# Optimization experiments

Measured on AMD Instinct MI355X. Metric: run time of the kernel, lower is better.

## Reference

```python
import jax, jax.numpy as jnp
import numpy as np


def _sepconv1x1(x, dw, pw, b):
    # SeparableConv2D with kernel=1: depthwise 1x1 = per-channel scale, then pointwise matmul
    return jnp.einsum('nhwc,cd->nhwd', x * dw, pw) + b


def setup_inputs() -> dict:
    key = jax.random.key(0)
    ks = jax.random.split(key, 12)
    N, H, W, C_in, C_red = 4, 64, 64, 256, 64
    s = 0.05  # small init so softmax logits are well-conditioned
    return {
        'feature_maps': jax.random.normal(ks[0], (N, H, W, C_in), jnp.float32),
        'global_channel_output': jax.random.normal(ks[1], (N, H, W, C_in), jnp.float32),
        'dw_q': jax.random.normal(ks[2], (C_in,), jnp.float32) * s,
        'pw_q': jax.random.normal(ks[3], (C_in, C_red), jnp.float32) * s,
        'b_q': jnp.zeros((C_red,), jnp.float32),
        'dw_k': jax.random.normal(ks[4], (C_in,), jnp.float32) * s,
        'pw_k': jax.random.normal(ks[5], (C_in, C_red), jnp.float32) * s,
        'b_k': jnp.zeros((C_red,), jnp.float32),
        'dw_v': jax.random.normal(ks[6], (C_in,), jnp.float32) * s,
        'pw_v': jax.random.normal(ks[7], (C_in, C_red), jnp.float32) * s,
        'b_v': jnp.zeros((C_red,), jnp.float32),
        'dw_a': jax.random.normal(ks[8], (C_red,), jnp.float32) * s,
        'pw_a': jax.random.normal(ks[9], (C_red, C_in), jnp.float32) * s,
        'b_a': jnp.zeros((C_in,), jnp.float32),
    }


def reference(feature_maps, global_channel_output,
              dw_q, pw_q, b_q, dw_k, pw_k, b_k, dw_v, pw_v, b_v,
              dw_a, pw_a, b_a):
    N, H, W, _ = feature_maps.shape
    q = _sepconv1x1(feature_maps, dw_q, pw_q, b_q)  # [N,H,W,Cr]
    k = _sepconv1x1(feature_maps, dw_k, pw_k, b_k)
    v = _sepconv1x1(feature_maps, dw_v, pw_v, b_v)
    Cr = q.shape[-1]
    q = q.reshape(N, H * W, Cr)
    k = k.reshape(N, H * W, Cr)
    v = v.reshape(N, H * W, Cr)
    # tf.matmul(key, query, transpose_b=True): scores[i,j] = key_i . query_j
    scores = jnp.einsum('nic,njc->nij', k, q)  # [N,HW,HW]
    scores = jax.nn.softmax(scores, axis=-1)
    # tf.matmul(value, scores, transpose_a=True) -> [N,Cr,HW]
    att = jnp.einsum('nic,nij->ncj', v, scores)
    # faithful raw reshape (as in the original TF code) from [N,Cr,HW] to [N,H,W,Cr]
    att = att.reshape(N, H, W, Cr)
    att = _sepconv1x1(att, dw_a, pw_a, b_a)  # [N,H,W,C_in]
    return global_channel_output * att + global_channel_output
```

## Files before the change

kernel.cpp:

```cpp
#include <hip/hip_runtime.h>
#include <hip/hip_bf16.h>

typedef __attribute__((ext_vector_type(8))) __bf16 bf16x8;
typedef __attribute__((ext_vector_type(2))) __bf16 bf16x2;
typedef __attribute__((ext_vector_type(4))) float floatx4;
typedef __attribute__((ext_vector_type(4))) unsigned short us4;
typedef __attribute__((ext_vector_type(8))) unsigned short us8;
typedef __attribute__((ext_vector_type(4))) short s16x4;
typedef __attribute__((ext_vector_type(2))) unsigned int uint2v;
typedef __attribute__((ext_vector_type(4))) unsigned int uint4v;

#define MFMA16(A, B, C) __builtin_amdgcn_mfma_f32_16x16x32_bf16((A), (B), (C), 0, 0, 0)
#define MFMA1K(A, B, C) __builtin_amdgcn_mfma_f32_16x16x16bf16_1k((A), (B), (C), 0, 0, 0)

#define LOG2E 1.44269504088896340736f

#if __has_builtin(__builtin_amdgcn_exp2f)
#define EXP2F(x) __builtin_amdgcn_exp2f(x)
#else
#define EXP2F(x) exp2f(x)
#endif

static __device__ __forceinline__ unsigned short f2bfbits(float f) {
    __hip_bfloat16 h = __float2bfloat16(f);
    union { __hip_bfloat16 h; unsigned short u; } cv;
    cv.h = h;
    return cv.u;
}
static __device__ __forceinline__ unsigned int rne32(float f) {
    unsigned int u = __builtin_bit_cast(unsigned int, f);
    return u + 0x7fffu + ((u >> 16) & 1u);
}
static __device__ __forceinline__ unsigned short rne16(float f) {
    return (unsigned short)(rne32(f) >> 16);
}

#if __has_builtin(__builtin_amdgcn_cvt_pk_bf16_f32)
static __device__ __forceinline__ s16x4 pack4(float e0, float e1, float e2, float e3) {
    bf16x2 lo = __builtin_amdgcn_cvt_pk_bf16_f32(e0, e1);
    bf16x2 hi = __builtin_amdgcn_cvt_pk_bf16_f32(e2, e3);
    uint2v u = {__builtin_bit_cast(unsigned int, lo), __builtin_bit_cast(unsigned int, hi)};
    return __builtin_bit_cast(s16x4, u);
}
static __device__ __forceinline__ bf16x8 cvt8(floatx4 a, floatx4 b) {
    bf16x2 p0 = __builtin_amdgcn_cvt_pk_bf16_f32(a[0], a[1]);
    bf16x2 p1 = __builtin_amdgcn_cvt_pk_bf16_f32(a[2], a[3]);
    bf16x2 p2 = __builtin_amdgcn_cvt_pk_bf16_f32(b[0], b[1]);
    bf16x2 p3 = __builtin_amdgcn_cvt_pk_bf16_f32(b[2], b[3]);
    uint4v u = {__builtin_bit_cast(unsigned int, p0), __builtin_bit_cast(unsigned int, p1),
                __builtin_bit_cast(unsigned int, p2), __builtin_bit_cast(unsigned int, p3)};
    return __builtin_bit_cast(bf16x8, u);
}
#else
static __device__ __forceinline__ s16x4 pack4(float e0, float e1, float e2, float e3) {
    unsigned int pa = __builtin_amdgcn_perm(rne32(e1), rne32(e0), 0x07060302u);
    unsigned int pb = __builtin_amdgcn_perm(rne32(e3), rne32(e2), 0x07060302u);
    uint2v u = {pa, pb};
    return __builtin_bit_cast(s16x4, u);
}
static __device__ __forceinline__ bf16x8 cvt8(floatx4 a, floatx4 b) {
    us8 u;
#pragma unroll
    for (int i = 0; i < 4; i++) { u[i] = rne16(a[i]); u[4 + i] = rne16(b[i]); }
    return __builtin_bit_cast(bf16x8, u);
}
#endif

static __device__ __forceinline__ bf16x8 load_bf8(const __hip_bfloat16* p) {
    return *reinterpret_cast<const bf16x8*>(p);
}
static __device__ __forceinline__ float bf2f(unsigned short u) {
    unsigned int w = ((unsigned int)u) << 16;
    return __builtin_bit_cast(float, w);
}


__global__ __launch_bounds__(256) void prep_w(
    const float* __restrict__ dwq, const float* __restrict__ pwq,
    const float* __restrict__ dwk, const float* __restrict__ pwk,
    const float* __restrict__ dwv, const float* __restrict__ pwv,
    __hip_bfloat16* __restrict__ wT)
{
    int idx = blockIdx.x * 256 + threadIdx.x;
    int p = idx >> 14;
    int r = idx & 16383;
    int d = r >> 8, c = r & 255;
    const float* dw = (p == 0) ? dwq : ((p == 1) ? dwk : dwv);
    const float* pw = (p == 0) ? pwq : ((p == 1) ? pwk : pwv);
    float scale = (p == 1) ? LOG2E : 1.0f;
    wT[idx] = __float2bfloat16(dw[c] * pw[c * 64 + d] * scale);
}

__global__ __launch_bounds__(256) void proj_qkv(
    const float* __restrict__ x,
    const __hip_bfloat16* __restrict__ wT,
    const float* __restrict__ bqp, const float* __restrict__ bkp,
    const float* __restrict__ bvp,
    __hip_bfloat16* __restrict__ qf, __hip_bfloat16* __restrict__ kf,
    __hip_bfloat16* __restrict__ vf)
{
    int wg = blockIdx.x * 4 + (threadIdx.x >> 6);
    int p = wg >> 10;
    int wid = wg & 1023;
    int lane = threadIdx.x & 63;
    int l15 = lane & 15, quad = lane >> 4;
    int strip = wid << 4;

    floatx4 acc[4];
#pragma unroll
    for (int t = 0; t < 4; t++) acc[t] = (floatx4){0.f, 0.f, 0.f, 0.f};

    const float* xrow = x + (strip + l15) * 256 + quad * 8;
    const __hip_bfloat16* wp = wT + p * 16384;
#pragma unroll
    for (int ks = 0; ks < 8; ks++) {
        floatx4 xa = *reinterpret_cast<const floatx4*>(xrow + ks * 32);
        floatx4 xb = *reinterpret_cast<const floatx4*>(xrow + ks * 32 + 4);
        bf16x8 a = cvt8(xa, xb);
#pragma unroll
        for (int t = 0; t < 4; t++) {
            bf16x8 b = load_bf8(wp + (t * 16 + l15) * 256 + ks * 32 + quad * 8);
            acc[t] = MFMA16(a, b, acc[t]);
        }
    }
    if (p < 2) {
        __hip_bfloat16* dst = (p == 0) ? qf : kf;
        const float* bias = (p == 0) ? bqp : bkp;
        float bscale = (p == 1) ? LOG2E : 1.0f;
#pragma unroll
        for (int t = 0; t < 4; t++) {
            float bsv = bias[t * 16 + l15] * bscale;
            int off0 = wid * 1024 + (t >> 1) * 512 +
                       (((((t & 1) << 1) | (l15 >> 3)) * 16 + quad * 4) * 8) + (l15 & 7);
#pragma unroll
            for (int r = 0; r < 4; r++)
                dst[off0 + r * 8] = __float2bfloat16(acc[t][r] + bsv);
        }
    } else {
#pragma unroll
        for (int t = 0; t < 4; t++) {
            float bsv = bvp[t * 16 + l15];
            us4 pk;
#pragma unroll
            for (int r = 0; r < 4; r++) pk[r] = f2bfbits(acc[t][r] + bsv);
            *reinterpret_cast<us4*>(vf + (wid * 4 + t) * 256 + lane * 4) = pk;
        }
    }
}

__global__ __launch_bounds__(512) void pass1_rl(
    const __hip_bfloat16* __restrict__ qf, const __hip_bfloat16* __restrict__ kf,
    const __hip_bfloat16* __restrict__ vf, __hip_bfloat16* __restrict__ vfs)
{
    int itg0 = blockIdx.x * 2;
    int n = itg0 >> 8;
    int jw = threadIdx.x >> 6;
    int lane = threadIdx.x & 63;
    int l15 = lane & 15, quad = lane >> 4;

    const __hip_bfloat16* kp = kf + itg0 * 1024 + lane * 8;
    bf16x8 a0 = load_bf8(kp);
    bf16x8 a1 = load_bf8(kp + 512);
    bf16x8 a2 = load_bf8(kp + 1024);
    bf16x8 a3 = load_bf8(kp + 1536);

    floatx4 lsA = (floatx4){0.f, 0.f, 0.f, 0.f};
    floatx4 lsB = (floatx4){0.f, 0.f, 0.f, 0.f};
    const __hip_bfloat16* qp0 = qf + (n * 256 + jw * 32) * 1024 + lane * 8;
    for (int it = 0; it < 16; it++, qp0 += 2048) {
        bf16x8 b0 = load_bf8(qp0);
        bf16x8 b1 = load_bf8(qp0 + 512);
        bf16x8 b2 = load_bf8(qp0 + 1024);
        bf16x8 b3 = load_bf8(qp0 + 1536);
        floatx4 z = (floatx4){0.f, 0.f, 0.f, 0.f};
        floatx4 sA0 = MFMA16(a1, b1, MFMA16(a0, b0, z));
        floatx4 sA1 = MFMA16(a1, b3, MFMA16(a0, b2, z));
        floatx4 sB0 = MFMA16(a3, b1, MFMA16(a2, b0, z));
        floatx4 sB1 = MFMA16(a3, b3, MFMA16(a2, b2, z));
#pragma unroll
        for (int r = 0; r < 4; r++) {
            lsA[r] += EXP2F(sA0[r]) + EXP2F(sA1[r]);
            lsB[r] += EXP2F(sB0[r]) + EXP2F(sB1[r]);
        }
    }
#pragma unroll
    for (int m = 1; m < 16; m <<= 1) {
#pragma unroll
        for (int r = 0; r < 4; r++) {
            lsA[r] += __shfl_xor(lsA[r], m, 64);
            lsB[r] += __shfl_xor(lsB[r], m, 64);
        }
    }
    __shared__ float red[8][32];
    __shared__ float rls[32];
    if (l15 == 0) {
#pragma unroll
        for (int r = 0; r < 4; r++) {
            red[jw][quad * 4 + r] = lsA[r];
            red[jw][16 + quad * 4 + r] = lsB[r];
        }
    }
    __syncthreads();
    if (threadIdx.x < 32) {
        float tot = 0.f;
#pragma unroll
        for (int w = 0; w < 8; w++) tot += red[w][threadIdx.x];
        rls[threadIdx.x] = 1.0f / tot;
    }
    __syncthreads();
    int m0 = threadIdx.x * 4;
    int toff = m0 >> 10;
    int mm = m0 & 1023;
    int t = mm >> 8;
    int l = (mm >> 2) & 63;
    int rb = toff * 16 + (l >> 4) * 4;
    us4 vv = *reinterpret_cast<const us4*>(
        reinterpret_cast<const unsigned short*>(vf) + itg0 * 1024 + m0);
    us4 ov;
#pragma unroll
    for (int r = 0; r < 4; r++) ov[r] = rne16(bf2f(vv[r]) * rls[rb + r]);
    *reinterpret_cast<us4*>(
        reinterpret_cast<unsigned short*>(vfs) + (itg0 + toff) * 1024 + l * 16 + t * 4) = ov;
}

template<int ITERS, int IHB>
__global__ __launch_bounds__(256) void pass2_att(
    const __hip_bfloat16* __restrict__ qf, const __hip_bfloat16* __restrict__ kf,
    const __hip_bfloat16* __restrict__ vfs,
    unsigned short* __restrict__ attp)
{
    int b = blockIdx.x;
    int ih = b & ((1 << IHB) - 1);
    int g = b >> IHB;
    int n = g >> 5;
    int jg = g & 31;
    int w = threadIdx.x >> 6;
    int jt0 = jg * 8 + w * 2;
    int lane = threadIdx.x & 63;
    int l15 = lane & 15, quad = lane >> 4;

    const __hip_bfloat16* qp = qf + (n * 256 + jt0) * 1024 + lane * 8;
    bf16x8 bq00 = load_bf8(qp);
    bf16x8 bq01 = load_bf8(qp + 512);
    bf16x8 bq10 = load_bf8(qp + 1024);
    bf16x8 bq11 = load_bf8(qp + 1536);

    floatx4 acc0[4], acc1[4];
#pragma unroll
    for (int t = 0; t < 4; t++) {
        acc0[t] = (floatx4){0.f, 0.f, 0.f, 0.f};
        acc1[t] = (floatx4){0.f, 0.f, 0.f, 0.f};
    }

    int it0 = n * 256 + ih * ITERS;
    const __hip_bfloat16* kp = kf + it0 * 1024 + lane * 8;
    const __hip_bfloat16* vp = vfs + it0 * 1024 + lane * 16;
    for (int it = 0; it < ITERS; it++, kp += 1024, vp += 1024) {
        bf16x8 a0 = load_bf8(kp);
        bf16x8 a1 = load_bf8(kp + 512);
        floatx4 z = (floatx4){0.f, 0.f, 0.f, 0.f};
        floatx4 s0 = MFMA16(a1, bq01, MFMA16(a0, bq00, z));
        floatx4 s1 = MFMA16(a1, bq11, MFMA16(a0, bq10, z));
        s16x4 p0 = pack4(EXP2F(s0[0]), EXP2F(s0[1]), EXP2F(s0[2]), EXP2F(s0[3]));
        s16x4 p1 = pack4(EXP2F(s1[0]), EXP2F(s1[1]), EXP2F(s1[2]), EXP2F(s1[3]));
        us8 v01 = *reinterpret_cast<const us8*>(vp);
        us8 v23 = *reinterpret_cast<const us8*>(vp + 8);
        s16x4 bv0 = __builtin_bit_cast(s16x4, __builtin_shufflevector(v01, v01, 0, 1, 2, 3));
        s16x4 bv1 = __builtin_bit_cast(s16x4, __builtin_shufflevector(v01, v01, 4, 5, 6, 7));
        s16x4 bv2 = __builtin_bit_cast(s16x4, __builtin_shufflevector(v23, v23, 0, 1, 2, 3));
        s16x4 bv3 = __builtin_bit_cast(s16x4, __builtin_shufflevector(v23, v23, 4, 5, 6, 7));
        acc0[0] = MFMA1K(p0, bv0, acc0[0]);
        acc1[0] = MFMA1K(p1, bv0, acc1[0]);
        acc0[1] = MFMA1K(p0, bv1, acc0[1]);
        acc1[1] = MFMA1K(p1, bv1, acc1[1]);
        acc0[2] = MFMA1K(p0, bv2, acc0[2]);
        acc1[2] = MFMA1K(p1, bv2, acc1[2]);
        acc0[3] = MFMA1K(p0, bv3, acc0[3]);
        acc1[3] = MFMA1K(p1, bv3, acc1[3]);
    }
    unsigned short* op0 = attp + ih * 1048576;
#pragma unroll
    for (int t = 0; t < 4; t++) {
        s16x4 k0 = pack4(acc0[t][0], acc0[t][1], acc0[t][2], acc0[t][3]);
        s16x4 k1 = pack4(acc1[t][0], acc1[t][1], acc1[t][2], acc1[t][3]);
        unsigned short* op = op0 + (n * 64 + t * 16 + l15) * 4096 + jt0 * 16 + quad * 4;
        *reinterpret_cast<s16x4*>(op) = k0;
        *reinterpret_cast<s16x4*>(op + 16) = k1;
    }
}

template<int NPART>
__global__ __launch_bounds__(256) void final_out(
    const unsigned short* __restrict__ attp, const float* __restrict__ gco,
    const float* __restrict__ dwa, const float* __restrict__ pwa,
    const float* __restrict__ ba, float* __restrict__ out)
{
    int b = blockIdx.x;
    int n = b >> 9;
    int hh = (b >> 3) & 63;
    int w0 = (b & 7) << 3;
    __shared__ float g[512];
    int tid = threadIdx.x;
    const unsigned short* ap = attp + (n * 64 + hh) * 4096 + w0 * 64;
    {
        int jj0 = tid * 2;
        float v0 = 0.f, v1 = 0.f;
#pragma unroll
        for (int ph = 0; ph < NPART; ph++) {
            unsigned int u = *reinterpret_cast<const unsigned int*>(ap + ph * 1048576 + jj0);
            v0 += bf2f((unsigned short)(u & 0xffffu));
            v1 += bf2f((unsigned short)(u >> 16));
        }
        g[jj0] = v0 * dwa[jj0 & 63];
        g[jj0 + 1] = v1 * dwa[(jj0 + 1) & 63];
    }
    __syncthreads();
    float acc[8];
#pragma unroll
    for (int w = 0; w < 8; w++) acc[w] = 0.f;
    for (int cc = 0; cc < 64; cc++) {
        float p = pwa[cc * 256 + tid];
#pragma unroll
        for (int w = 0; w < 8; w++) acc[w] += g[w * 64 + cc] * p;
    }
    float bb = ba[tid];
#pragma unroll
    for (int w = 0; w < 8; w++) {
        int pos = (n * 64 + hh) * 64 + w0 + w;
        float gv = gco[pos * 256 + tid];
        out[pos * 256 + tid] = gv * (acc[w] + bb) + gv;
    }
}

extern "C" void kernel_launch(void* const* d_in, const int* in_sizes, int n_in,
                              void* d_out, int out_size, void* d_ws, size_t ws_size,
                              hipStream_t stream) {
    const float* x   = (const float*)d_in[0];
    const float* gco = (const float*)d_in[1];
    const float* dwq = (const float*)d_in[2];
    const float* pwq = (const float*)d_in[3];
    const float* bq  = (const float*)d_in[4];
    const float* dwk = (const float*)d_in[5];
    const float* pwk = (const float*)d_in[6];
    const float* bk  = (const float*)d_in[7];
    const float* dwv = (const float*)d_in[8];
    const float* pwv = (const float*)d_in[9];
    const float* bv  = (const float*)d_in[10];
    const float* dwa = (const float*)d_in[11];
    const float* pwa = (const float*)d_in[12];
    const float* ba  = (const float*)d_in[13];
    float* out = (float*)d_out;

    char* ws = (char*)d_ws;
    __hip_bfloat16* wT  = (__hip_bfloat16*)ws;
    __hip_bfloat16* qf  = (__hip_bfloat16*)(ws + 98304);
    __hip_bfloat16* kf  = (__hip_bfloat16*)(ws + 2195456);
    __hip_bfloat16* vf  = (__hip_bfloat16*)(ws + 4292608);
    __hip_bfloat16* vfs = (__hip_bfloat16*)(ws + 6389760);
    unsigned short* attp = (unsigned short*)(ws + 8486912);

    const size_t NEED16 = 8486912u + 16u * 2097152u;

    prep_w<<<192, 256, 0, stream>>>(dwq, pwq, dwk, pwk, dwv, pwv, wT);
    proj_qkv<<<768, 256, 0, stream>>>(x, wT, bq, bk, bv, qf, kf, vf);
    pass1_rl<<<512, 512, 0, stream>>>(qf, kf, vf, vfs);
    if (ws_size >= NEED16) {
        pass2_att<16, 4><<<2048, 256, 0, stream>>>(qf, kf, vfs, attp);
        final_out<16><<<2048, 256, 0, stream>>>(attp, gco, dwa, pwa, ba, out);
    } else {
        pass2_att<32, 3><<<1024, 256, 0, stream>>>(qf, kf, vfs, attp);
        final_out<8><<<2048, 256, 0, stream>>>(attp, gco, dwa, pwa, ba, out);
    }
}
```

Measured before the change: 182.6 us.

## Widen pass2 query tile per wave, prefetch K/V, use fewer i-partitions

Each wave now handles four query tiles instead of two, so every loaded K/V tile feeds twice as many MFMAs, and the next iteration's K and V tiles are prefetched into registers. The launch always uses the 8-partition variant with 512 blocks, removing the 16-partition path and halving the partial buffers that final_out reduces. This cuts global K/V traffic and the final reduction work, but uses more registers per thread and launches fewer blocks, which may lower occupancy and latency hiding.

```diff
diff --git a/kernel.cpp b/kernel.cpp
--- a/kernel.cpp
+++ b/kernel.cpp
@@ -232,60 +232,95 @@
     int b = blockIdx.x;
     int ih = b & ((1 << IHB) - 1);
     int g = b >> IHB;
-    int n = g >> 5;
-    int jg = g & 31;
+    int n = g >> 4;
+    int jg = g & 15;
     int w = threadIdx.x >> 6;
-    int jt0 = jg * 8 + w * 2;
+    int jt0 = jg * 16 + w * 4;
     int lane = threadIdx.x & 63;
     int l15 = lane & 15, quad = lane >> 4;
 
     const __hip_bfloat16* qp = qf + (n * 256 + jt0) * 1024 + lane * 8;
-    bf16x8 bq00 = load_bf8(qp);
-    bf16x8 bq01 = load_bf8(qp + 512);
-    bf16x8 bq10 = load_bf8(qp + 1024);
-    bf16x8 bq11 = load_bf8(qp + 1536);
-
-    floatx4 acc0[4], acc1[4];
+    bf16x8 bq0a = load_bf8(qp);
+    bf16x8 bq0b = load_bf8(qp + 512);
+    bf16x8 bq1a = load_bf8(qp + 1024);
+    bf16x8 bq1b = load_bf8(qp + 1536);
+    bf16x8 bq2a = load_bf8(qp + 2048);
+    bf16x8 bq2b = load_bf8(qp + 2560);
+    bf16x8 bq3a = load_bf8(qp + 3072);
+    bf16x8 bq3b = load_bf8(qp + 3584);
+
+    floatx4 acc0[4], acc1[4], acc2[4], acc3[4];
 #pragma unroll
     for (int t = 0; t < 4; t++) {
         acc0[t] = (floatx4){0.f, 0.f, 0.f, 0.f};
         acc1[t] = (floatx4){0.f, 0.f, 0.f, 0.f};
+        acc2[t] = (floatx4){0.f, 0.f, 0.f, 0.f};
+        acc3[t] = (floatx4){0.f, 0.f, 0.f, 0.f};
     }
 
     int it0 = n * 256 + ih * ITERS;
     const __hip_bfloat16* kp = kf + it0 * 1024 + lane * 8;
     const __hip_bfloat16* vp = vfs + it0 * 1024 + lane * 16;
-    for (int it = 0; it < ITERS; it++, kp += 1024, vp += 1024) {
-        bf16x8 a0 = load_bf8(kp);
-        bf16x8 a1 = load_bf8(kp + 512);
+
+    bf16x8 a0 = load_bf8(kp);
+    bf16x8 a1 = load_bf8(kp + 512);
+    us8 v01 = *reinterpret_cast<const us8*>(vp);
+    us8 v23 = *reinterpret_cast<const us8*>(vp + 8);
+
+    for (int it = 0; it < ITERS; it++) {
+        bf16x8 na0, na1; us8 nv01, nv23;
+        if (it + 1 < ITERS) {
+            const __hip_bfloat16* kpn = kp + 1024;
+            const __hip_bfloat16* vpn = vp + 1024;
+            na0 = load_bf8(kpn);
+            na1 = load_bf8(kpn + 512);
+            nv01 = *reinterpret_cast<const us8*>(vpn);
+            nv23 = *reinterpret_cast<const us8*>(vpn + 8);
+        }
         floatx4 z = (floatx4){0.f, 0.f, 0.f, 0.f};
-        floatx4 s0 = MFMA16(a1, bq01, MFMA16(a0, bq00, z));
-        floatx4 s1 = MFMA16(a1, bq11, MFMA16(a0, bq10, z));
+        floatx4 s0 = MFMA16(a1, bq0b, MFMA16(a0, bq0a, z));
+        floatx4 s1 = MFMA16(a1, bq1b, MFMA16(a0, bq1a, z));
+        floatx4 s2 = MFMA16(a1, bq2b, MFMA16(a0, bq2a, z));
+        floatx4 s3 = MFMA16(a1, bq3b, MFMA16(a0, bq3a, z));
         s16x4 p0 = pack4(EXP2F(s0[0]), EXP2F(s0[1]), EXP2F(s0[2]), EXP2F(s0[3]));
         s16x4 p1 = pack4(EXP2F(s1[0]), EXP2F(s1[1]), EXP2F(s1[2]), EXP2F(s1[3]));
-        us8 v01 = *reinterpret_cast<const us8*>(vp);
-        us8 v23 = *reinterpret_cast<const us8*>(vp + 8);
+        s16x4 p2 = pack4(EXP2F(s2[0]), EXP2F(s2[1]), EXP2F(s2[2]), EXP2F(s2[3]));
+        s16x4 p3 = pack4(EXP2F(s3[0]), EXP2F(s3[1]), EXP2F(s3[2]), EXP2F(s3[3]));
         s16x4 bv0 = __builtin_bit_cast(s16x4, __builtin_shufflevector(v01, v01, 0, 1, 2, 3));
         s16x4 bv1 = __builtin_bit_cast(s16x4, __builtin_shufflevector(v01, v01, 4, 5, 6, 7));
         s16x4 bv2 = __builtin_bit_cast(s16x4, __builtin_shufflevector(v23, v23, 0, 1, 2, 3));
         s16x4 bv3 = __builtin_bit_cast(s16x4, __builtin_shufflevector(v23, v23, 4, 5, 6, 7));
         acc0[0] = MFMA1K(p0, bv0, acc0[0]);
         acc1[0] = MFMA1K(p1, bv0, acc1[0]);
+        acc2[0] = MFMA1K(p2, bv0, acc2[0]);
+        acc3[0] = MFMA1K(p3, bv0, acc3[0]);
         acc0[1] = MFMA1K(p0, bv1, acc0[1]);
         acc1[1] = MFMA1K(p1, bv1, acc1[1]);
+        acc2[1] = MFMA1K(p2, bv1, acc2[1]);
+        acc3[1] = MFMA1K(p3, bv1, acc3[1]);
         acc0[2] = MFMA1K(p0, bv2, acc0[2]);
         acc1[2] = MFMA1K(p1, bv2, acc1[2]);
+        acc2[2] = MFMA1K(p2, bv2, acc2[2]);
+        acc3[2] = MFMA1K(p3, bv2, acc3[2]);
         acc0[3] = MFMA1K(p0, bv3, acc0[3]);
         acc1[3] = MFMA1K(p1, bv3, acc1[3]);
+        acc2[3] = MFMA1K(p2, bv3, acc2[3]);
+        acc3[3] = MFMA1K(p3, bv3, acc3[3]);
+        a0 = na0; a1 = na1; v01 = nv01; v23 = nv23;
+        kp += 1024; vp += 1024;
     }
     unsigned short* op0 = attp + ih * 1048576;
 #pragma unroll
     for (int t = 0; t < 4; t++) {
         s16x4 k0 = pack4(acc0[t][0], acc0[t][1], acc0[t][2], acc0[t][3]);
         s16x4 k1 = pack4(acc1[t][0], acc1[t][1], acc1[t][2], acc1[t][3]);
+        s16x4 k2 = pack4(acc2[t][0], acc2[t][1], acc2[t][2], acc2[t][3]);
+        s16x4 k3 = pack4(acc3[t][0], acc3[t][1], acc3[t][2], acc3[t][3]);
         unsigned short* op = op0 + (n * 64 + t * 16 + l15) * 4096 + jt0 * 16 + quad * 4;
         *reinterpret_cast<s16x4*>(op) = k0;
         *reinterpret_cast<s16x4*>(op + 16) = k1;
+        *reinterpret_cast<s16x4*>(op + 32) = k2;
+        *reinterpret_cast<s16x4*>(op + 48) = k3;
     }
 }
 
@@ -359,16 +394,9 @@
     __hip_bfloat16* vfs = (__hip_bfloat16*)(ws + 6389760);
     unsigned short* attp = (unsigned short*)(ws + 8486912);
 
-    const size_t NEED16 = 8486912u + 16u * 2097152u;
-
     prep_w<<<192, 256, 0, stream>>>(dwq, pwq, dwk, pwk, dwv, pwv, wT);
     proj_qkv<<<768, 256, 0, stream>>>(x, wT, bq, bk, bv, qf, kf, vf);
     pass1_rl<<<512, 512, 0, stream>>>(qf, kf, vf, vfs);
-    if (ws_size >= NEED16) {
-        pass2_att<16, 4><<<2048, 256, 0, stream>>>(qf, kf, vfs, attp);
-        final_out<16><<<2048, 256, 0, stream>>>(attp, gco, dwa, pwa, ba, out);
-    } else {
-        pass2_att<32, 3><<<1024, 256, 0, stream>>>(qf, kf, vfs, attp);
-        final_out<8><<<2048, 256, 0, stream>>>(attp, gco, dwa, pwa, ba, out);
-    }
-}
+    pass2_att<32, 3><<<512, 256, 0, stream>>>(qf, kf, vfs, attp);
+    final_out<8><<<2048, 256, 0, stream>>>(attp, gco, dwa, pwa, ba, out);
+}
```

After: 177.4 us. -2.8%, faster.
